# Kernel optimization log

Measured on AMD Instinct MI355X. Metric: run time of the kernel, lower is better.

## Reference

```python
import jax, jax.numpy as jnp
import numpy as np

B, N, L, E, U, G, R, D, C = 64, 50000, 8, 100000, 20000, 20000, 64, 16, 2


def setup_inputs() -> dict:
    rng = np.random.default_rng(0)
    key = jax.random.key(0)
    ks = jax.random.split(key, 10)
    # index structures (duplicate-free where the torch code assumes uniqueness)
    gene_map = jnp.asarray(rng.choice(N, G, replace=False).astype(np.int32))
    dst_unique = jnp.stack([jnp.asarray(rng.choice(N, U, replace=False).astype(np.int32)) for _ in range(L)])
    root_ids = jnp.asarray(rng.choice(N, R, replace=False).astype(np.int32))
    src = jax.random.randint(ks[0], (L, E), 0, N, dtype=jnp.int32)
    dst_pos = jax.random.randint(ks[1], (L, E), 0, U, dtype=jnp.int32)
    # data and parameters
    X_gene_batch = jax.random.normal(ks[2], (B, G), jnp.float32)
    w_in = jax.random.normal(ks[3], (D,), jnp.float32) * 0.5   # Linear(1, d) weight
    b_in = jax.random.normal(ks[4], (D,), jnp.float32) * 0.1
    W = jax.random.normal(ks[5], (L, D, D), jnp.float32) * (1.0 / np.sqrt(D))  # xavier-ish
    bias = jnp.zeros((N, D), jnp.float32)
    W_head = jax.random.normal(ks[6], (C, R * D), jnp.float32) * (1.0 / np.sqrt(R * D))
    b_head = jnp.zeros((C,), jnp.float32)
    return {
        "X_gene_batch": X_gene_batch, "w_in": w_in, "b_in": b_in, "W": W,
        "bias": bias, "W_head": W_head, "b_head": b_head,
        "gene_map": gene_map, "src": src, "dst_pos": dst_pos,
        "dst_unique": dst_unique, "root_ids": root_ids,
    }


def reference(X_gene_batch, w_in, b_in, W, bias, W_head, b_head,
              gene_map, src, dst_pos, dst_unique, root_ids):
    Bn = X_gene_batch.shape[0]
    n_nodes, d = bias.shape
    n_layers = W.shape[0]
    u = dst_unique.shape[1]
    # _init_state_vector: h=0, scatter in_proj(X[...,None]) at gene_map
    gene_emb = X_gene_batch[..., None] * w_in + b_in          # [B, G, d]
    h = jnp.zeros((Bn, n_nodes, d), X_gene_batch.dtype)
    h = h.at[:, gene_map].set(gene_emb)
    for li in range(n_layers):
        h_src = h[:, src[li]]                                  # gather [B, E, d]
        msg = jnp.einsum('bed,df->bef', h_src, W[li])          # small dxd matmul
        agg = jnp.zeros((Bn, u, d), h.dtype).at[:, dst_pos[li]].add(msg)  # scatter-add
        h_dst = jnp.tanh(agg + bias[dst_unique[li]][None])     # bias lookup + tanh (dropout=0)
        h = h.at[:, dst_unique[li]].set(h_dst)                 # write back
    feat = h[:, root_ids].reshape(Bn, -1)                      # roots_concat readout
    return feat @ W_head.T + b_head                            # [B, C]
```

## Files before the change

### kernel.cpp

```cpp
#include <hip/hip_runtime.h>
#include <hip/hip_fp16.h>
#include <cmath>

constexpr int B_ = 64, N_ = 50000, L_ = 8, E_ = 100000, U_ = 20000, G_ = 20000, R_ = 64, D_ = 16, C_ = 2;
constexpr int EPL_ = E_ + 3 * U_ + 4096;
constexpr int EPLG_ = EPL_ / 4 + 64;
constexpr int GPW = 8;
constexpr int GCAP = EPL_ / 4;
constexpr int SW = (GCAP + GPW - 1) / GPW;
constexpr int HISTB = (E_ + 255) / 256;

constexpr int BC = 64;
constexpr int F = BC * 2;

constexpr int HBC = 32;
constexpr int FH = HBC * 2;
constexpr int DST0 = 1 + G_;
constexpr int AROWS = DST0 + L_ * U_;

__device__ __forceinline__ float tanh_fast(float x) {
  float e = __expf(2.0f * x);
  return 1.0f - 2.0f * __builtin_amdgcn_rcpf(e + 1.0f);
}


__global__ __launch_bounds__(256) void hist_mark_k(
    const int* __restrict__ dst_pos, int* __restrict__ cnt,
    int* __restrict__ rank, const int* __restrict__ dst_unique,
    const int* __restrict__ gene_map, int* __restrict__ wmask,
    int* __restrict__ posarr, int* __restrict__ lw0) {
  int li = blockIdx.y;
  int bx = blockIdx.x;
  if (bx < HISTB) {
    int e = bx * 256 + threadIdx.x;
    if (e < E_)
      rank[li * E_ + e] = atomicAdd(&cnt[li * U_ + dst_pos[li * E_ + e]], 1);
  } else if (li == 0) {
    int t = (bx - HISTB) * 256 + threadIdx.x;
    if (t < L_ * U_) {
      int lj = t / U_, u = t % U_;
      int n = dst_unique[t];
      posarr[lj * N_ + n] = u;
      atomicOr(&wmask[n], 1 << lj);
    } else {
      int g = t - L_ * U_;
      if (g < G_) lw0[gene_map[g]] = 1 + g;
    }
  }
}

__global__ __launch_bounds__(1024) void scan_kernel(
    const int* __restrict__ cnt, int* __restrict__ offs) {
  __shared__ int sums[1024];
  int li = blockIdx.x, t = threadIdx.x;
  int base = t * 20;
  int v[20];
  int s = 0;
#pragma unroll
  for (int i = 0; i < 20; ++i) {
    int idx = base + i;
    int c = (idx < U_) ? cnt[li * U_ + idx] : -1;
    int pc = (c < 0) ? 0 : ((c == 0) ? 4 : ((c + 3) & ~3));
    v[i] = s;
    s += pc;
  }
  sums[t] = s;
  __syncthreads();
  for (int off = 1; off < 1024; off <<= 1) {
    int o = (t >= off) ? sums[t - off] : 0;
    __syncthreads();
    sums[t] += o;
    __syncthreads();
  }
  int excl = sums[t] - s;
#pragma unroll
  for (int i = 0; i < 20; ++i) {
    int idx = base + i;
    if (idx < U_) offs[li * (U_ + 1) + idx] = excl + v[i];
  }
  if (t == 1023) offs[li * (U_ + 1) + U_] = sums[1023];
}

__global__ __launch_bounds__(256) void scatter_kernel(
    const int* __restrict__ dst_pos, const int* __restrict__ src,
    const int* __restrict__ offs, const int* __restrict__ rank,
    int* __restrict__ ssrc) {
  int e = blockIdx.x * 256 + threadIdx.x;
  int li = blockIdx.y;
  if (e >= E_) return;
  int u = dst_pos[li * E_ + e];
  int p = offs[li * (U_ + 1) + u] + rank[li * E_ + e];
  ssrc[(size_t)li * EPL_ + p] = src[li * E_ + e];
}

__global__ __launch_bounds__(256) void pad_fill_ug_k(
    const int* __restrict__ cnt, const int* __restrict__ offs,
    int* __restrict__ ssrc, int* __restrict__ ug, float4* __restrict__ zrow) {
  int t = blockIdx.x * 256 + threadIdx.x;
  if (t < L_ * U_) {
    int li = t / U_, u = t % U_;
    int start = offs[li * (U_ + 1) + u];
    int end = start + cnt[li * U_ + u];
    int pend = offs[li * (U_ + 1) + u + 1];
    int* sp = ssrc + (size_t)li * EPL_;
    for (int p = end; p < pend; ++p) sp[p] = N_;
    int* ugp = ug + (size_t)li * EPLG_;
    for (int g = start >> 2; g < (pend >> 2); ++g) ugp[g] = u;
  } else {
    int t2 = t - L_ * U_;
    int li = t2 >> 10, j = t2 & 1023;
    if (li < L_) {
      int* sp = ssrc + (size_t)li * EPL_;
      int ptot = offs[li * (U_ + 1) + U_];
      if (j < 256) {
        int pos = ptot + j;
        if (pos < EPL_) sp[pos] = N_;
        sp[EPL_ - 256 + j] = N_;
      }
      int* ugp = ug + (size_t)li * EPLG_;
      for (int gq = (ptot >> 2) + j; gq < EPLG_; gq += 1024) ugp[gq] = -1;
      if (li == 0 && j < FH && zrow) zrow[j] = make_float4(0.f, 0.f, 0.f, 0.f);
    }
  }
}

__global__ __launch_bounds__(256) void remap_k(
    const int* __restrict__ offs, const int* __restrict__ wmask,
    const int* __restrict__ posarr, const int* __restrict__ lw0,
    int* __restrict__ ssrc) {
  int p = blockIdx.x * 256 + threadIdx.x;
  int li = blockIdx.y;
  if (p >= EPL_) return;
  int ptot = offs[li * (U_ + 1) + U_];
  if (p >= ptot + 256 && p < EPL_ - 256) return;
  int* sp = ssrc + (size_t)li * EPL_;
  int s = sp[p];
  int m = wmask[s] & ((1 << li) - 1);
  int phys;
  if (m) {
    int lj = 31 - __clz(m);
    phys = DST0 + lj * U_ + posarr[lj * N_ + s];
  } else {
    phys = lw0[s];
  }
  sp[p] = phys;
}

#define PHASE(VACC, VLD, IDLD, IDPF, NUCUR)          \
  {                                                  \
    loadRows(VLD, IDLD);                             \
    IDPF = *(const int4*)(sp + 4 * CLG(g + 4));      \
    int nuCur = NUCUR;                               \
    NUCUR = ugp[CLG(g + 3) + 1];                     \
    accum(VACC);                                     \
    if (nuCur != curU) {                             \
      flushu(curU);                                  \
      if (g + 1 >= gstop) return;                    \
      curU = nuCur;                                  \
    }                                                \
    ++g;                                             \
  }


__global__ __launch_bounds__(256) void gene_a(
    const float* __restrict__ X, const float* __restrict__ w_in,
    const float* __restrict__ b_in, float4* __restrict__ h4, int half) {
  __shared__ float xs[8][33];
  int tid = threadIdx.x;
  int g0 = blockIdx.x * 8;
  {
    int b = tid >> 3, gi = tid & 7;
    xs[gi][b] = X[(size_t)(half * HBC + b) * G_ + g0 + gi];
  }
  __syncthreads();
  int b = tid & 31;
  int gi = tid >> 5;
  float x = xs[gi][b];
  int g = g0 + gi;
  float4 out[2];
  __half2* oh = reinterpret_cast<__half2*>(out);
#pragma unroll
  for (int k = 0; k < 8; ++k) {
    float r0 = fmaf(x, w_in[2 * k], b_in[2 * k]);
    float r1 = fmaf(x, w_in[2 * k + 1], b_in[2 * k + 1]);
    oh[k] = __float22half2_rn(make_float2(r0, r1));
  }
  h4[(size_t)(1 + g) * FH + b * 2] = out[0];
  h4[(size_t)(1 + g) * FH + b * 2 + 1] = out[1];
}

__global__ __launch_bounds__(256, 2) void gfused_a(
    const float4* __restrict__ h4, const int* __restrict__ ug,
    const int* __restrict__ ssrc, const float* __restrict__ W,
    const float* __restrict__ bias, const int* __restrict__ dst_unique,
    float4* __restrict__ o4, int li) {
  __shared__ float Wlds[256];
  int tid = threadIdx.x;
  Wlds[tid] = W[li * 256 + tid];
  __syncthreads();
  int lane = tid & 63;
  int dh = lane & 1;
  int wv = __builtin_amdgcn_readfirstlane(blockIdx.x * 4 + (tid >> 6));
  const int* ugp = ug + (size_t)li * EPLG_;
  const int* sp = ssrc + (size_t)li * EPL_;
  const int* du = dst_unique + (size_t)li * U_;

  int g0 = wv * GPW, gend = g0 + GPW;
  int prevU = (g0 == 0) ? -2 : ugp[g0 - 1];
  int g = g0;
  while (g < gend && ugp[g] == prevU) ++g;
  if (g >= gend) return;
  int curU = ugp[g];
  if (curU < 0) return;
  int uend = ugp[gend - 1];
  int gstop;
  if (uend < 0) {
    gstop = g;
    while (ugp[gstop] >= 0) ++gstop;
  } else {
    gstop = gend;
    while (ugp[gstop] == uend) ++gstop;
  }

  __half2 acc[2][4];
  const __half2 z = __half2half2(__float2half(0.f));
#pragma unroll
  for (int j = 0; j < 2; ++j)
#pragma unroll
    for (int k = 0; k < 4; ++k) acc[j][k] = z;

  auto flushu = [&](int u) {
    int node = du[u];
    float biasv[8];
    {
      const float4* bp = (const float4*)(bias + (size_t)node * 16 + dh * 8);
      float4 q0 = bp[0], q1 = bp[1];
      biasv[0] = q0.x; biasv[1] = q0.y; biasv[2] = q0.z; biasv[3] = q0.w;
      biasv[4] = q1.x; biasv[5] = q1.y; biasv[6] = q1.z; biasv[7] = q1.w;
    }
    float a8[8];
#pragma unroll
    for (int k = 0; k < 4; ++k) {
      float2 f0 = __half22float2(acc[0][k]);
      float2 f1 = __half22float2(acc[1][k]);
      __half2 hv = __float22half2_rn(make_float2(f0.x + f1.x, f0.y + f1.y));
      float2 fa = __half22float2(hv);
      a8[2 * k] = fa.x; a8[2 * k + 1] = fa.y;
    }
    float pm[16];
#pragma unroll
    for (int j = 0; j < 16; ++j) pm[j] = 0.f;
#pragma unroll
    for (int dd = 0; dd < 8; ++dd) {
      float s = a8[dd];
      const float4* wr = (const float4*)&Wlds[(dh * 8 + dd) * 16];
      float4 w0 = wr[0], w1 = wr[1], w2 = wr[2], w3 = wr[3];
      pm[0] = fmaf(s, w0.x, pm[0]);  pm[1] = fmaf(s, w0.y, pm[1]);
      pm[2] = fmaf(s, w0.z, pm[2]);  pm[3] = fmaf(s, w0.w, pm[3]);
      pm[4] = fmaf(s, w1.x, pm[4]);  pm[5] = fmaf(s, w1.y, pm[5]);
      pm[6] = fmaf(s, w1.z, pm[6]);  pm[7] = fmaf(s, w1.w, pm[7]);
      pm[8] = fmaf(s, w2.x, pm[8]);  pm[9] = fmaf(s, w2.y, pm[9]);
      pm[10] = fmaf(s, w2.z, pm[10]); pm[11] = fmaf(s, w2.w, pm[11]);
      pm[12] = fmaf(s, w3.x, pm[12]); pm[13] = fmaf(s, w3.y, pm[13]);
      pm[14] = fmaf(s, w3.z, pm[14]); pm[15] = fmaf(s, w3.w, pm[15]);
    }
    float m8[8];
#pragma unroll
    for (int jj = 0; jj < 8; ++jj) {
      float s0 = pm[jj] + __shfl_xor(pm[jj], 1, 64);
      float s1 = pm[8 + jj] + __shfl_xor(pm[8 + jj], 1, 64);
      m8[jj] = dh ? s1 : s0;
    }
    float4 outv;
    __half2* ov = reinterpret_cast<__half2*>(&outv);
#pragma unroll
    for (int k = 0; k < 4; ++k) {
      ov[k] = __float22half2_rn(
          make_float2(tanh_fast(m8[2 * k] + biasv[2 * k]),
                      tanh_fast(m8[2 * k + 1] + biasv[2 * k + 1])));
    }
    o4[(size_t)(DST0 + li * U_ + u) * FH + lane] = outv;
#pragma unroll
    for (int j = 0; j < 2; ++j)
#pragma unroll
      for (int k = 0; k < 4; ++k) acc[j][k] = z;
  };

  auto loadRows = [&](float4 (&v)[4], int4 id) {
    v[0] = h4[(size_t)id.x * FH + lane];
    v[1] = h4[(size_t)id.y * FH + lane];
    v[2] = h4[(size_t)id.z * FH + lane];
    v[3] = h4[(size_t)id.w * FH + lane];
  };
  auto accum = [&](const float4 (&v)[4]) {
#pragma unroll
    for (int j = 0; j < 4; ++j) {
      const __half2* p = reinterpret_cast<const __half2*>(&v[j]);
#pragma unroll
      for (int k = 0; k < 4; ++k)
        acc[j & 1][k] = __hadd2(acc[j & 1][k], p[k]);
    }
  };
  auto CLG = [&](int q) { return (q < GCAP) ? q : GCAP - 1; };

  int4 id0 = *(const int4*)(sp + 4 * g);
  int4 id1 = *(const int4*)(sp + 4 * CLG(g + 1));
  int4 idP = *(const int4*)(sp + 4 * CLG(g + 2));
  int4 idQ = *(const int4*)(sp + 4 * CLG(g + 3));
  int4 idR;
  int nuA = ugp[g + 1];
  int nuB = ugp[CLG(g + 1) + 1];
  int nuC = ugp[CLG(g + 2) + 1];

  float4 va[4], vb[4], vc[4];
  loadRows(va, id0);
  loadRows(vb, id1);

  for (;;) {
    PHASE(va, vc, idP, idR, nuA)
    PHASE(vb, va, idQ, idP, nuB)
    PHASE(vc, vb, idR, idQ, nuC)
  }
}

__global__ __launch_bounds__(64) void head_a(
    const float4* __restrict__ h4, const float* __restrict__ W_head,
    const float* __restrict__ b_head, const int* __restrict__ root_ids,
    const int* __restrict__ wmask, const int* __restrict__ posarr,
    const int* __restrict__ lw0, int half, float* __restrict__ out) {
  int bl = blockIdx.x;
  int r = threadIdx.x;
  int node = root_ids[r];
  int m = wmask[node];
  int phys;
  if (m) {
    int lj = 31 - __clz(m);
    phys = DST0 + lj * U_ + posarr[lj * N_ + node];
  } else {
    phys = lw0[node];
  }
  float4 p0 = h4[(size_t)phys * FH + bl * 2];
  float4 p1 = h4[(size_t)phys * FH + bl * 2 + 1];
  float v[16];
  const __half2* ph0 = reinterpret_cast<const __half2*>(&p0);
  const __half2* ph1 = reinterpret_cast<const __half2*>(&p1);
#pragma unroll
  for (int k = 0; k < 4; ++k) {
    float2 f0 = __half22float2(ph0[k]);
    float2 f1 = __half22float2(ph1[k]);
    v[2 * k] = f0.x; v[2 * k + 1] = f0.y;
    v[8 + 2 * k] = f1.x; v[8 + 2 * k + 1] = f1.y;
  }
  float acc0 = 0.f, acc1 = 0.f;
#pragma unroll
  for (int d = 0; d < 16; ++d) {
    acc0 = fmaf(v[d], W_head[r * 16 + d], acc0);
    acc1 = fmaf(v[d], W_head[1024 + r * 16 + d], acc1);
  }
  for (int off = 32; off; off >>= 1) {
    acc0 += __shfl_down(acc0, off, 64);
    acc1 += __shfl_down(acc1, off, 64);
  }
  if (r == 0) {
    int gb = half * HBC + bl;
    out[gb * 2 + 0] = acc0 + b_head[0];
    out[gb * 2 + 1] = acc1 + b_head[1];
  }
}


__global__ __launch_bounds__(256) void gene_c(
    const float* __restrict__ X, const float* __restrict__ w_in,
    const float* __restrict__ b_in, const int* __restrict__ gene_map,
    float4* __restrict__ h4) {
  int t = blockIdx.x * 256 + threadIdx.x;
  if (t >= G_ * BC) return;
  int b = t % BC;
  int g = t / BC;
  float x = X[b * G_ + g];
  int node = gene_map[g];
  float4 out[2];
  __half2* oh = reinterpret_cast<__half2*>(out);
#pragma unroll
  for (int k = 0; k < 8; ++k) {
    float r0 = fmaf(x, w_in[2 * k], b_in[2 * k]);
    float r1 = fmaf(x, w_in[2 * k + 1], b_in[2 * k + 1]);
    oh[k] = __float22half2_rn(make_float2(r0, r1));
  }
  h4[(size_t)node * F + b * 2] = out[0];
  h4[(size_t)node * F + b * 2 + 1] = out[1];
}

__global__ __launch_bounds__(256, 2) void gather_c(
    const float4* __restrict__ h4, const int* __restrict__ ug,
    const int* __restrict__ ssrc, float4* __restrict__ agg4, int li) {
  int tid = threadIdx.x;
  int lane = tid & 63;
  int wv = __builtin_amdgcn_readfirstlane(blockIdx.x * 4 + (tid >> 6));
  const int* ugp = ug + (size_t)li * EPLG_;
  const int* sp = ssrc + (size_t)li * EPL_;

  int g0 = wv * GPW, gend = g0 + GPW;
  int prevU = (g0 == 0) ? -2 : ugp[g0 - 1];
  int g = g0;
  while (g < gend && ugp[g] == prevU) ++g;
  if (g >= gend) return;
  int curU = ugp[g];
  if (curU < 0) return;
  int uend = ugp[gend - 1];
  int gstop;
  if (uend < 0) {
    gstop = g;
    while (ugp[gstop] >= 0) ++gstop;
  } else {
    gstop = gend;
    while (ugp[gstop] == uend) ++gstop;
  }

  __half2 acc[2][2][4];
  const __half2 z = __half2half2(__float2half(0.f));
#pragma unroll
  for (int j = 0; j < 2; ++j)
#pragma unroll
    for (int r = 0; r < 2; ++r)
#pragma unroll
      for (int k = 0; k < 4; ++k) acc[j][r][k] = z;

  auto flushu = [&](int u) {
#pragma unroll
    for (int r = 0; r < 2; ++r) {
      float4 outv;
      __half2* ov = reinterpret_cast<__half2*>(&outv);
#pragma unroll
      for (int k = 0; k < 4; ++k) {
        float2 f0 = __half22float2(acc[0][r][k]);
        float2 f1 = __half22float2(acc[1][r][k]);
        ov[k] = __float22half2_rn(make_float2(f0.x + f1.x, f0.y + f1.y));
      }
      agg4[(size_t)u * F + lane + r * 64] = outv;
    }
#pragma unroll
    for (int j = 0; j < 2; ++j)
#pragma unroll
      for (int r = 0; r < 2; ++r)
#pragma unroll
        for (int k = 0; k < 4; ++k) acc[j][r][k] = z;
  };
  auto loadRows = [&](float4 (&v)[4][2], int4 id) {
    v[0][0] = h4[(size_t)id.x * F + lane]; v[0][1] = h4[(size_t)id.x * F + lane + 64];
    v[1][0] = h4[(size_t)id.y * F + lane]; v[1][1] = h4[(size_t)id.y * F + lane + 64];
    v[2][0] = h4[(size_t)id.z * F + lane]; v[2][1] = h4[(size_t)id.z * F + lane + 64];
    v[3][0] = h4[(size_t)id.w * F + lane]; v[3][1] = h4[(size_t)id.w * F + lane + 64];
  };
  auto accum = [&](const float4 (&v)[4][2]) {
#pragma unroll
    for (int j = 0; j < 4; ++j)
#pragma unroll
      for (int r = 0; r < 2; ++r) {
        const __half2* p = reinterpret_cast<const __half2*>(&v[j][r]);
#pragma unroll
        for (int k = 0; k < 4; ++k)
          acc[j & 1][r][k] = __hadd2(acc[j & 1][r][k], p[k]);
      }
  };
  auto CLG = [&](int q) { return (q < GCAP) ? q : GCAP - 1; };

  int4 id0 = *(const int4*)(sp + 4 * g);
  int4 id1 = *(const int4*)(sp + 4 * CLG(g + 1));
  int4 idP = *(const int4*)(sp + 4 * CLG(g + 2));
  int4 idQ = *(const int4*)(sp + 4 * CLG(g + 3));
  int4 idR;
  int nuA = ugp[g + 1];
  int nuB = ugp[CLG(g + 1) + 1];
  int nuC = ugp[CLG(g + 2) + 1];

  float4 va[4][2], vb[4][2], vc[4][2];
  loadRows(va, id0);
  loadRows(vb, id1);

  for (;;) {
    PHASE(va, vc, idP, idR, nuA)
    PHASE(vb, va, idQ, idP, nuB)
    PHASE(vc, vb, idR, idQ, nuC)
  }
}
#undef PHASE

__global__ __launch_bounds__(256) void dense_c(
    const float4* __restrict__ agg4, const float* __restrict__ W,
    const float* __restrict__ bias, const int* __restrict__ dst_unique,
    float4* __restrict__ h4, int li) {
  __shared__ float Wlds[256];
  int tid = threadIdx.x;
  Wlds[tid] = W[li * 256 + tid];
  __syncthreads();
  int u = __builtin_amdgcn_readfirstlane(blockIdx.x * 4 + (tid >> 6));
  int b = tid & 63;
  float4 c0 = agg4[(size_t)u * F + b * 2];
  float4 c1 = agg4[(size_t)u * F + b * 2 + 1];
  float a[16];
  {
    const __half2* p0 = reinterpret_cast<const __half2*>(&c0);
    const __half2* p1 = reinterpret_cast<const __half2*>(&c1);
#pragma unroll
    for (int k = 0; k < 4; ++k) {
      float2 f0 = __half22float2(p0[k]);
      float2 f1 = __half22float2(p1[k]);
      a[2 * k] = f0.x; a[2 * k + 1] = f0.y;
      a[8 + 2 * k] = f1.x; a[8 + 2 * k + 1] = f1.y;
    }
  }
  float m[16];
#pragma unroll
  for (int j = 0; j < 16; ++j) m[j] = 0.f;
#pragma unroll
  for (int d = 0; d < 16; ++d) {
    float s = a[d];
    const float4* wr = (const float4*)&Wlds[d * 16];
    float4 w0 = wr[0], w1 = wr[1], w2 = wr[2], w3 = wr[3];
    m[0] = fmaf(s, w0.x, m[0]);  m[1] = fmaf(s, w0.y, m[1]);
    m[2] = fmaf(s, w0.z, m[2]);  m[3] = fmaf(s, w0.w, m[3]);
    m[4] = fmaf(s, w1.x, m[4]);  m[5] = fmaf(s, w1.y, m[5]);
    m[6] = fmaf(s, w1.z, m[6]);  m[7] = fmaf(s, w1.w, m[7]);
    m[8] = fmaf(s, w2.x, m[8]);  m[9] = fmaf(s, w2.y, m[9]);
    m[10] = fmaf(s, w2.z, m[10]); m[11] = fmaf(s, w2.w, m[11]);
    m[12] = fmaf(s, w3.x, m[12]); m[13] = fmaf(s, w3.y, m[13]);
    m[14] = fmaf(s, w3.z, m[14]); m[15] = fmaf(s, w3.w, m[15]);
  }
  int node = dst_unique[li * U_ + u];
  const float4* bp = (const float4*)(bias + (size_t)node * 16);
  float4 b0 = bp[0], b1 = bp[1], b2 = bp[2], b3 = bp[3];
  float bb[16] = {b0.x, b0.y, b0.z, b0.w, b1.x, b1.y, b1.z, b1.w,
                  b2.x, b2.y, b2.z, b2.w, b3.x, b3.y, b3.z, b3.w};
  float4 o0, o1;
  __half2* ov0 = reinterpret_cast<__half2*>(&o0);
  __half2* ov1 = reinterpret_cast<__half2*>(&o1);
#pragma unroll
  for (int k = 0; k < 4; ++k) {
    ov0[k] = __float22half2_rn(make_float2(tanh_fast(m[2 * k] + bb[2 * k]),
                                           tanh_fast(m[2 * k + 1] + bb[2 * k + 1])));
    ov1[k] = __float22half2_rn(make_float2(tanh_fast(m[8 + 2 * k] + bb[8 + 2 * k]),
                                           tanh_fast(m[8 + 2 * k + 1] + bb[8 + 2 * k + 1])));
  }
  h4[(size_t)node * F + b * 2] = o0;
  h4[(size_t)node * F + b * 2 + 1] = o1;
}

__global__ __launch_bounds__(64) void head_c(
    const float4* __restrict__ h4, const float* __restrict__ W_head,
    const float* __restrict__ b_head, const int* __restrict__ root_ids,
    float* __restrict__ out) {
  int bl = blockIdx.x;
  int r = threadIdx.x;
  int node = root_ids[r];
  float4 p0 = h4[(size_t)node * F + bl * 2];
  float4 p1 = h4[(size_t)node * F + bl * 2 + 1];
  float v[16];
  const __half2* ph0 = reinterpret_cast<const __half2*>(&p0);
  const __half2* ph1 = reinterpret_cast<const __half2*>(&p1);
#pragma unroll
  for (int k = 0; k < 4; ++k) {
    float2 f0 = __half22float2(ph0[k]);
    float2 f1 = __half22float2(ph1[k]);
    v[2 * k] = f0.x; v[2 * k + 1] = f0.y;
    v[8 + 2 * k] = f1.x; v[8 + 2 * k + 1] = f1.y;
  }
  float acc0 = 0.f, acc1 = 0.f;
#pragma unroll
  for (int d = 0; d < 16; ++d) {
    acc0 = fmaf(v[d], W_head[r * 16 + d], acc0);
    acc1 = fmaf(v[d], W_head[1024 + r * 16 + d], acc1);
  }
  for (int off = 32; off; off >>= 1) {
    acc0 += __shfl_down(acc0, off, 64);
    acc1 += __shfl_down(acc1, off, 64);
  }
  if (r == 0) {
    out[bl * 2 + 0] = acc0 + b_head[0];
    out[bl * 2 + 1] = acc1 + b_head[1];
  }
}

__global__ void zero_out_k(float* out, int n) {
  int t = blockIdx.x * 256 + threadIdx.x;
  if (t < n) out[t] = 0.f;
}


static size_t arena_bytes() {
  return (size_t)AROWS * FH * 16 +
         (size_t)L_ * U_ * 4 +
         (size_t)2 * (N_ + 1) * 4 +
         (size_t)L_ * (U_ + 1) * 4 +
         (size_t)L_ * E_ * 4 +
         (size_t)L_ * EPL_ * 4 +
         (size_t)L_ * EPLG_ * 4 +
         (size_t)L_ * N_ * 4;
}
static size_t classic_bytes() {
  return (size_t)(N_ + 1) * F * 16 + (size_t)U_ * F * 16 +
         (size_t)L_ * U_ * 4 + (size_t)L_ * (U_ + 1) * 4 +
         (size_t)L_ * E_ * 4 + (size_t)L_ * EPL_ * 4 + (size_t)L_ * EPLG_ * 4;
}

extern "C" void kernel_launch(void* const* d_in, const int* in_sizes, int n_in,
                              void* d_out, int out_size, void* d_ws, size_t ws_size,
                              hipStream_t stream) {
  const float* X = (const float*)d_in[0];
  const float* w_in = (const float*)d_in[1];
  const float* b_in = (const float*)d_in[2];
  const float* W = (const float*)d_in[3];
  const float* bias = (const float*)d_in[4];
  const float* W_head = (const float*)d_in[5];
  const float* b_head = (const float*)d_in[6];
  const int* gene_map = (const int*)d_in[7];
  const int* src = (const int*)d_in[8];
  const int* dst_pos = (const int*)d_in[9];
  const int* dst_unique = (const int*)d_in[10];
  const int* root_ids = (const int*)d_in[11];
  float* out = (float*)d_out;

  dim3 egrid(HISTB, L_);
  const int pf_grid = (L_ * U_ + L_ * 1024 + 255) / 256;
  const int gather_grid = (SW + 3) / 4;

  if (ws_size >= arena_bytes()) {
    char* ws = (char*)d_ws;
    float4* arena = (float4*)ws;
    size_t off = (size_t)AROWS * FH * 16;
    int* cnt = (int*)(ws + off);    off += (size_t)L_ * U_ * 4;
    int* wmask = (int*)(ws + off);  off += (size_t)(N_ + 1) * 4;
    int* lw0 = (int*)(ws + off);    off += (size_t)(N_ + 1) * 4;
    int* offs = (int*)(ws + off);   off += (size_t)L_ * (U_ + 1) * 4;
    int* rank = (int*)(ws + off);   off += (size_t)L_ * E_ * 4;
    int* ssrc = (int*)(ws + off);   off += (size_t)L_ * EPL_ * 4;
    int* ug = (int*)(ws + off);     off += (size_t)L_ * EPLG_ * 4;
    int* posarr = (int*)(ws + off);

    hipMemsetAsync(cnt, 0, (size_t)L_ * U_ * 4 + (size_t)2 * (N_ + 1) * 4,
                   stream);
    dim3 hmgrid(HISTB + (L_ * U_ + G_ + 255) / 256, L_);
    hist_mark_k<<<hmgrid, 256, 0, stream>>>(dst_pos, cnt, rank, dst_unique,
                                            gene_map, wmask, posarr, lw0);
    scan_kernel<<<L_, 1024, 0, stream>>>(cnt, offs);
    scatter_kernel<<<egrid, 256, 0, stream>>>(dst_pos, src, offs, rank, ssrc);
    pad_fill_ug_k<<<pf_grid, 256, 0, stream>>>(cnt, offs, ssrc, ug, arena);
    dim3 rgrid((EPL_ + 255) / 256, L_);
    remap_k<<<rgrid, 256, 0, stream>>>(offs, wmask, posarr, lw0, ssrc);

    for (int half = 0; half < 2; ++half) {
      gene_a<<<G_ / 8, 256, 0, stream>>>(X, w_in, b_in, arena, half);
      for (int li = 0; li < L_; ++li) {
        gfused_a<<<gather_grid, 256, 0, stream>>>(arena, ug, ssrc, W, bias,
                                                  dst_unique, arena, li);
      }
      head_a<<<HBC, 64, 0, stream>>>(arena, W_head, b_head, root_ids, wmask,
                                     posarr, lw0, half, out);
    }
  } else if (ws_size >= classic_bytes()) {
    const size_t h_bytes = (size_t)(N_ + 1) * F * 16;
    const size_t agg_bytes = (size_t)U_ * F * 16;
    char* ws = (char*)d_ws;
    float4* h4 = (float4*)ws;
    float4* agg4 = (float4*)(ws + h_bytes);
    size_t off = h_bytes + agg_bytes;
    int* cnt = (int*)(ws + off);   off += (size_t)L_ * U_ * 4;
    int* offs = (int*)(ws + off);  off += (size_t)L_ * (U_ + 1) * 4;
    int* rank = (int*)(ws + off);  off += (size_t)L_ * E_ * 4;
    int* ssrc = (int*)(ws + off);  off += (size_t)L_ * EPL_ * 4;
    int* ug = (int*)(ws + off);

    hipMemsetAsync(cnt, 0, (size_t)L_ * U_ * 4, stream);
    hipMemsetAsync(h4, 0, h_bytes, stream);
    hist_mark_k<<<egrid, 256, 0, stream>>>(dst_pos, cnt, rank, nullptr,
                                           nullptr, nullptr, nullptr, nullptr);
    scan_kernel<<<L_, 1024, 0, stream>>>(cnt, offs);
    scatter_kernel<<<egrid, 256, 0, stream>>>(dst_pos, src, offs, rank, ssrc);
    pad_fill_ug_k<<<pf_grid, 256, 0, stream>>>(cnt, offs, ssrc, ug, nullptr);
    gene_c<<<(G_ * BC + 255) / 256, 256, 0, stream>>>(X, w_in, b_in, gene_map, h4);
    const int dense_grid = U_ * BC / 256;
    for (int li = 0; li < L_; ++li) {
      gather_c<<<gather_grid, 256, 0, stream>>>(h4, ug, ssrc, agg4, li);
      dense_c<<<dense_grid, 256, 0, stream>>>(agg4, W, bias, dst_unique, h4, li);
    }
    head_c<<<BC, 64, 0, stream>>>(h4, W_head, b_head, root_ids, out);
  } else {
    zero_out_k<<<(out_size + 255) / 256, 256, 0, stream>>>(out, out_size);
  }
}
```

Baseline: 553.0 us.

## Replace global-atomic destination histogram with LDS-privatized per-block partial counts

The per-layer counting-sort histogram over dst_pos moves from global atomics to shared-memory atomics. Each of 32 edge blocks builds a private histogram in two halves of the destination range to fit in LDS. A new pass turns the per-block counts into prefix bases and totals, and scatter adds the block base to the local rank while handling four edges per thread. The node-marking work is split into its own kernel. This removes global atomic contention in the preprocessing but adds a partial-count buffer, an extra pass over it and extra launches.

```diff
diff --git a/kernel.cpp b/kernel.cpp
--- a/kernel.cpp
+++ b/kernel.cpp
@@ -8,7 +8,10 @@
 constexpr int GPW = 8;
 constexpr int GCAP = EPL_ / 4;
 constexpr int SW = (GCAP + GPW - 1) / GPW;
-constexpr int HISTB = (E_ + 255) / 256;
+
+constexpr int NB = 32;
+constexpr int EB = E_ / NB;
+constexpr int URB = U_ / 2;
 
 constexpr int BC = 64;
 constexpr int F = BC * 2;
@@ -24,29 +27,45 @@
 }
 
 
-__global__ __launch_bounds__(256) void hist_mark_k(
-    const int* __restrict__ dst_pos, int* __restrict__ cnt,
-    int* __restrict__ rank, const int* __restrict__ dst_unique,
-    const int* __restrict__ gene_map, int* __restrict__ wmask,
-    int* __restrict__ posarr, int* __restrict__ lw0) {
+__global__ __launch_bounds__(256) void hist_lds_k(
+    const int* __restrict__ dst_pos, int* __restrict__ rank,
+    int* __restrict__ part) {
+  __shared__ int hcnt[URB];
+  int li = blockIdx.y, b = blockIdx.x;
+  int tid = threadIdx.x;
+  int e0 = b * EB, e1 = e0 + EB;
+  const int* dp = dst_pos + (size_t)li * E_;
+  int* rk = rank + (size_t)li * E_;
+#pragma unroll
+  for (int r = 0; r < 2; ++r) {
+    int ub = r * URB;
+    for (int i = tid; i < URB; i += 256) hcnt[i] = 0;
+    __syncthreads();
+    for (int e = e0 + tid; e < e1; e += 256) {
+      int u = dp[e] - ub;
+      if ((unsigned)u < (unsigned)URB) rk[e] = atomicAdd(&hcnt[u], 1);
+    }
+    __syncthreads();
+    int* pp = part + ((size_t)li * NB + b) * U_ + ub;
+    for (int i = tid; i < URB; i += 256) pp[i] = hcnt[i];
+    __syncthreads();
+  }
+}
+
+__global__ __launch_bounds__(256) void sumpart_k(
+    int* __restrict__ part, int* __restrict__ cnt) {
+  int u = blockIdx.x * 256 + threadIdx.x;
   int li = blockIdx.y;
-  int bx = blockIdx.x;
-  if (bx < HISTB) {
-    int e = bx * 256 + threadIdx.x;
-    if (e < E_)
-      rank[li * E_ + e] = atomicAdd(&cnt[li * U_ + dst_pos[li * E_ + e]], 1);
-  } else if (li == 0) {
-    int t = (bx - HISTB) * 256 + threadIdx.x;
-    if (t < L_ * U_) {
-      int lj = t / U_, u = t % U_;
-      int n = dst_unique[t];
-      posarr[lj * N_ + n] = u;
-      atomicOr(&wmask[n], 1 << lj);
-    } else {
-      int g = t - L_ * U_;
-      if (g < G_) lw0[gene_map[g]] = 1 + g;
-    }
-  }
+  if (u >= U_) return;
+  int s = 0;
+#pragma unroll 4
+  for (int b = 0; b < NB; ++b) {
+    size_t idx = ((size_t)li * NB + b) * U_ + u;
+    int v = part[idx];
+    part[idx] = s;
+    s += v;
+  }
+  cnt[li * U_ + u] = s;
 }
 
 __global__ __launch_bounds__(1024) void scan_kernel(
@@ -83,14 +102,23 @@
 
 __global__ __launch_bounds__(256) void scatter_kernel(
     const int* __restrict__ dst_pos, const int* __restrict__ src,
-    const int* __restrict__ offs, const int* __restrict__ rank,
-    int* __restrict__ ssrc) {
-  int e = blockIdx.x * 256 + threadIdx.x;
+    const int* __restrict__ offs, const int* __restrict__ part,
+    const int* __restrict__ rank, int* __restrict__ ssrc) {
+  int e4 = (blockIdx.x * 256 + threadIdx.x) * 4;
   int li = blockIdx.y;
-  if (e >= E_) return;
-  int u = dst_pos[li * E_ + e];
-  int p = offs[li * (U_ + 1) + u] + rank[li * E_ + e];
-  ssrc[(size_t)li * EPL_ + p] = src[li * E_ + e];
+  if (e4 >= E_) return;
+  int4 dp = *(const int4*)(dst_pos + (size_t)li * E_ + e4);
+  int4 rk = *(const int4*)(rank + (size_t)li * E_ + e4);
+  int4 sv = *(const int4*)(src + (size_t)li * E_ + e4);
+  const int* op = offs + li * (U_ + 1);
+  const int* pb = part + (size_t)li * NB * U_;
+  int* sp = ssrc + (size_t)li * EPL_;
+  int b0 = (e4 + 0) / EB, b1 = (e4 + 1) / EB;
+  int b2 = (e4 + 2) / EB, b3 = (e4 + 3) / EB;
+  sp[op[dp.x] + pb[(size_t)b0 * U_ + dp.x] + rk.x] = sv.x;
+  sp[op[dp.y] + pb[(size_t)b1 * U_ + dp.y] + rk.y] = sv.y;
+  sp[op[dp.z] + pb[(size_t)b2 * U_ + dp.z] + rk.z] = sv.z;
+  sp[op[dp.w] + pb[(size_t)b3 * U_ + dp.w] + rk.w] = sv.w;
 }
 
 __global__ __launch_bounds__(256) void pad_fill_ug_k(
@@ -124,6 +152,21 @@
   }
 }
 
+__global__ __launch_bounds__(256) void mark_k(
+    const int* __restrict__ dst_unique, const int* __restrict__ gene_map,
+    int* __restrict__ wmask, int* __restrict__ posarr, int* __restrict__ lw0) {
+  int t = blockIdx.x * 256 + threadIdx.x;
+  if (t < L_ * U_) {
+    int li = t / U_, u = t % U_;
+    int n = dst_unique[t];
+    posarr[li * N_ + n] = u;
+    atomicOr(&wmask[n], 1 << li);
+  } else {
+    int g = t - L_ * U_;
+    if (g < G_) lw0[gene_map[g]] = 1 + g;
+  }
+}
+
 __global__ __launch_bounds__(256) void remap_k(
     const int* __restrict__ offs, const int* __restrict__ wmask,
     const int* __restrict__ posarr, const int* __restrict__ lw0,
@@ -593,6 +636,7 @@
          (size_t)2 * (N_ + 1) * 4 +
          (size_t)L_ * (U_ + 1) * 4 +
          (size_t)L_ * E_ * 4 +
+         (size_t)L_ * NB * U_ * 4 +
          (size_t)L_ * EPL_ * 4 +
          (size_t)L_ * EPLG_ * 4 +
          (size_t)L_ * N_ * 4;
@@ -600,7 +644,8 @@
 static size_t classic_bytes() {
   return (size_t)(N_ + 1) * F * 16 + (size_t)U_ * F * 16 +
          (size_t)L_ * U_ * 4 + (size_t)L_ * (U_ + 1) * 4 +
-         (size_t)L_ * E_ * 4 + (size_t)L_ * EPL_ * 4 + (size_t)L_ * EPLG_ * 4;
+         (size_t)L_ * E_ * 4 + (size_t)L_ * NB * U_ * 4 +
+         (size_t)L_ * EPL_ * 4 + (size_t)L_ * EPLG_ * 4;
 }
 
 extern "C" void kernel_launch(void* const* d_in, const int* in_sizes, int n_in,
@@ -620,7 +665,9 @@
   const int* root_ids = (const int*)d_in[11];
   float* out = (float*)d_out;
 
-  dim3 egrid(HISTB, L_);
+  dim3 hgrid(NB, L_);
+  dim3 spgrid((U_ + 255) / 256, L_);
+  dim3 scgrid((E_ / 4 + 255) / 256, L_);
   const int pf_grid = (L_ * U_ + L_ * 1024 + 255) / 256;
   const int gather_grid = (SW + 3) / 4;
 
@@ -633,18 +680,20 @@
     int* lw0 = (int*)(ws + off);    off += (size_t)(N_ + 1) * 4;
     int* offs = (int*)(ws + off);   off += (size_t)L_ * (U_ + 1) * 4;
     int* rank = (int*)(ws + off);   off += (size_t)L_ * E_ * 4;
+    int* part = (int*)(ws + off);   off += (size_t)L_ * NB * U_ * 4;
     int* ssrc = (int*)(ws + off);   off += (size_t)L_ * EPL_ * 4;
     int* ug = (int*)(ws + off);     off += (size_t)L_ * EPLG_ * 4;
     int* posarr = (int*)(ws + off);
 
-    hipMemsetAsync(cnt, 0, (size_t)L_ * U_ * 4 + (size_t)2 * (N_ + 1) * 4,
-                   stream);
-    dim3 hmgrid(HISTB + (L_ * U_ + G_ + 255) / 256, L_);
-    hist_mark_k<<<hmgrid, 256, 0, stream>>>(dst_pos, cnt, rank, dst_unique,
-                                            gene_map, wmask, posarr, lw0);
+    hipMemsetAsync(wmask, 0, (size_t)2 * (N_ + 1) * 4, stream);
+    hist_lds_k<<<hgrid, 256, 0, stream>>>(dst_pos, rank, part);
+    sumpart_k<<<spgrid, 256, 0, stream>>>(part, cnt);
     scan_kernel<<<L_, 1024, 0, stream>>>(cnt, offs);
-    scatter_kernel<<<egrid, 256, 0, stream>>>(dst_pos, src, offs, rank, ssrc);
+    scatter_kernel<<<scgrid, 256, 0, stream>>>(dst_pos, src, offs, part, rank,
+                                               ssrc);
     pad_fill_ug_k<<<pf_grid, 256, 0, stream>>>(cnt, offs, ssrc, ug, arena);
+    mark_k<<<(L_ * U_ + G_ + 255) / 256, 256, 0, stream>>>(dst_unique, gene_map,
+                                                           wmask, posarr, lw0);
     dim3 rgrid((EPL_ + 255) / 256, L_);
     remap_k<<<rgrid, 256, 0, stream>>>(offs, wmask, posarr, lw0, ssrc);
 
@@ -667,15 +716,16 @@
     int* cnt = (int*)(ws + off);   off += (size_t)L_ * U_ * 4;
     int* offs = (int*)(ws + off);  off += (size_t)L_ * (U_ + 1) * 4;
     int* rank = (int*)(ws + off);  off += (size_t)L_ * E_ * 4;
+    int* part = (int*)(ws + off);  off += (size_t)L_ * NB * U_ * 4;
     int* ssrc = (int*)(ws + off);  off += (size_t)L_ * EPL_ * 4;
     int* ug = (int*)(ws + off);
 
-    hipMemsetAsync(cnt, 0, (size_t)L_ * U_ * 4, stream);
     hipMemsetAsync(h4, 0, h_bytes, stream);
-    hist_mark_k<<<egrid, 256, 0, stream>>>(dst_pos, cnt, rank, nullptr,
-                                           nullptr, nullptr, nullptr, nullptr);
+    hist_lds_k<<<hgrid, 256, 0, stream>>>(dst_pos, rank, part);
+    sumpart_k<<<spgrid, 256, 0, stream>>>(part, cnt);
     scan_kernel<<<L_, 1024, 0, stream>>>(cnt, offs);
-    scatter_kernel<<<egrid, 256, 0, stream>>>(dst_pos, src, offs, rank, ssrc);
+    scatter_kernel<<<scgrid, 256, 0, stream>>>(dst_pos, src, offs, part, rank,
+                                               ssrc);
     pad_fill_ug_k<<<pf_grid, 256, 0, stream>>>(cnt, offs, ssrc, ug, nullptr);
     gene_c<<<(G_ * BC + 255) / 256, 256, 0, stream>>>(X, w_in, b_in, gene_map, h4);
     const int dense_grid = U_ * BC / 256;
```

Result: no change. 552.8 us (-0.0%).
